# Performance work log

Hardware: AMD Instinct MI355X
Metric: run time of the kernel (lower is better)

The kernel has to match this reference:

```python
import jax, jax.numpy as jnp
import numpy as np
from jax import lax

B, C, H, W = 8, 64, 256, 256
K = 10  # num_experts


def conv1x1(x, w):
    # x: [B,C,H,W], w: [O,C] (1x1 conv, no bias)
    return jnp.einsum('oc,bchw->bohw', w, x)


def dyn_conv_se(x, attn, Wk, bk, gamma):
    # Dynamic_conv2d_se with with_se=True, kernel 3, stride 1, pad 1, groups=1.
    # attn: [B,K]; Wk: [K,O,I,3,3]; bk: [K,O]; gamma: [B,O]
    aw = jnp.einsum('bk,koihw->boihw', attn, Wk)        # per-sample kernels
    ab = attn @ bk                                      # [B,O]

    def one(xi, wi):
        # xi: [C,H,W], wi: [O,I,3,3]
        return lax.conv_general_dilated(
            xi[None], wi, window_strides=(1, 1), padding='SAME',
            dimension_numbers=('NCHW', 'OIHW', 'NCHW'))[0]

    y = jax.vmap(one)(x, aw) + ab[:, :, None, None]
    return y * gamma[:, :, None, None]  # SE gain


def setup_inputs() -> dict:
    key = jax.random.key(0)
    ks = jax.random.split(key, 12)
    x = jax.random.normal(ks[0], (B, C, H, W), dtype=jnp.float32)
    logits = jax.random.uniform(ks[1], (B, K), dtype=jnp.float32)
    weights = jax.nn.softmax(logits, axis=-1)
    gamma = jax.random.uniform(ks[2], (B, C), dtype=jnp.float32)
    par = jax.random.uniform(ks[3], (B, 3, 1, H, W), dtype=jnp.float32)
    s = 0.1  # default_init_weights scale
    w1 = jax.random.normal(ks[4], (K, C, C, 3, 3), dtype=jnp.float32) * s
    b1 = jax.random.normal(ks[5], (K, C), dtype=jnp.float32) * 0.01
    w2 = jax.random.normal(ks[6], (K, C, C, 3, 3), dtype=jnp.float32) * s
    b2 = jax.random.normal(ks[7], (K, C), dtype=jnp.float32) * 0.01
    w_16x16 = jax.random.normal(ks[8], (C, C), dtype=jnp.float32) * s
    w_16x8 = jax.random.normal(ks[9], (C, C), dtype=jnp.float32) * s
    w_8x8 = jax.random.normal(ks[10], (C, C), dtype=jnp.float32) * s
    return {'x': x, 'weights': weights, 'gamma': gamma, 'par': par,
            'w1': w1, 'b1': b1, 'w2': w2, 'b2': b2,
            'w_16x16': w_16x16, 'w_16x8': w_16x8, 'w_8x8': w_8x8}


def reference(x, weights, gamma, par, w1, b1, w2, b2, w_16x16, w_16x8, w_8x8):
    # channel_first=True, sparse_val=False, one_layer=False, res_scale=1
    identity = x
    dyres = (conv1x1(x, w_16x16) * par[:, 0]
             + conv1x1(x, w_16x8) * par[:, 1]
             + conv1x1(x, w_8x8) * par[:, 2])
    out = jax.nn.relu(dyn_conv_se(x, weights, w2, b2, gamma) + dyres)
    out = dyn_conv_se(out, weights, w1, b1, gamma)
    return identity + out  # res_scale = 1
```

## Files before the change

### kernel.cpp

```cpp
#include <hip/hip_runtime.h>
#include <hip/hip_bf16.h>

typedef __attribute__((ext_vector_type(8))) short short8;
typedef __attribute__((ext_vector_type(4))) float f32x4;

#define B_ 8
#define C_ 64
#define H_ 256
#define W_ 256
#define HW_ 65536
#define K_ 10
#define NS1 24
#define NS2 18
#define HP_ 258
#define WP_ 258
#define PXP_ (HP_*WP_)
#define SLABW 34
#define SLABR 10

static __device__ __forceinline__ unsigned short f2bf(float f) {
    __hip_bfloat16 hb = __float2bfloat16(f);
    return *(unsigned short*)&hb;
}
static __device__ __forceinline__ float bf2f(unsigned short u) {
    unsigned v = ((unsigned)u) << 16;
    float f;
    __builtin_memcpy(&f, &v, 4);
    return f;
}

static __device__ __forceinline__ void gload_lds16(const void* g, void* l) {
    __builtin_amdgcn_global_load_lds(
        (const __attribute__((address_space(1))) unsigned int*)(unsigned long long)g,
        (__attribute__((address_space(3))) unsigned int*)(unsigned int)(unsigned long long)l,
        16, 0, 0);
}

__global__ void k_combine(const float* __restrict__ attn, const float* __restrict__ gamma,
                          const float* __restrict__ w1, const float* __restrict__ b1,
                          const float* __restrict__ w2, const float* __restrict__ b2,
                          const float* __restrict__ w16, const float* __restrict__ w168,
                          const float* __restrict__ w88,
                          unsigned short* __restrict__ W4_1, unsigned short* __restrict__ W4_2,
                          float* __restrict__ bias1, float* __restrict__ bias2) {
    const int N1 = B_ * NS1 * 2048;
    const int N2 = B_ * NS2 * 2048;
    int gid = blockIdx.x * 256 + threadIdx.x;
    if (gid < N1) {
        int b = gid / (NS1 * 2048);
        int r = gid - b * (NS1 * 2048);
        int s = r >> 11;
        int r2 = r & 2047;
        int of = r2 >> 9, l = (r2 >> 3) & 63, j = r2 & 7;
        int o = of * 16 + (l & 15);
        int g = l >> 4;
        float val;
        if (s < 18) {
            int t = s >> 1, h = s & 1;
            int c = h * 32 + g * 8 + j;
            float acc = 0.f;
            #pragma unroll
            for (int k = 0; k < K_; ++k)
                acc += attn[b * K_ + k] * w2[((size_t)(k * 64 + o) * 64 + c) * 9 + t];
            val = acc * gamma[b * 64 + o];
        } else {
            int e = s - 18;
            int m = e >> 1, h = e & 1;
            int c = h * 32 + g * 8 + j;
            const float* wm = (m == 0) ? w16 : (m == 1 ? w168 : w88);
            val = wm[o * 64 + c];
        }
        W4_1[gid] = f2bf(val);
    } else if (gid < N1 + N2) {
        int gid2 = gid - N1;
        int b = gid2 / (NS2 * 2048);
        int r = gid2 - b * (NS2 * 2048);
        int s = r >> 11;
        int r2 = r & 2047;
        int of = r2 >> 9, l = (r2 >> 3) & 63, j = r2 & 7;
        int o = of * 16 + (l & 15);
        int g = l >> 4;
        int t = s >> 1, h = s & 1;
        int c = h * 32 + g * 8 + j;
        float acc = 0.f;
        #pragma unroll
        for (int k = 0; k < K_; ++k)
            acc += attn[b * K_ + k] * w1[((size_t)(k * 64 + o) * 64 + c) * 9 + t];
        W4_2[gid2] = f2bf(acc * gamma[b * 64 + o]);
    } else if (gid < N1 + N2 + 1024) {
        int id2 = gid - N1 - N2;
        int b = id2 >> 7;
        int rest = id2 & 127;
        int o = rest >> 1;
        int which = rest & 1;
        const float* bb = which ? b1 : b2;
        float acc = 0.f;
        #pragma unroll
        for (int k = 0; k < K_; ++k) acc += attn[b * K_ + k] * bb[k * 64 + o];
        float v = acc * gamma[b * 64 + o];
        if (which) bias2[b * 64 + o] = v; else bias1[b * 64 + o] = v;
    }
}

__global__ void k_border(unsigned short* __restrict__ X1p, unsigned short* __restrict__ Tp) {
    int gid = blockIdx.x * 256 + threadIdx.x;
    if (gid >= 2 * B_ * 1028 * 8) return;
    int chunk = gid & 7;
    int rest = gid >> 3;
    int p = rest % 1028;
    int rb = rest / 1028;
    int buf = rb & 1, b = rb >> 1;
    int row, col;
    if (p < 258) { row = 0; col = p; }
    else if (p < 516) { row = 257; col = p - 258; }
    else if (p < 772) { row = p - 516 + 1; col = 0; }
    else { row = p - 772 + 1; col = 257; }
    unsigned short* base = (buf ? Tp : X1p) +
        ((size_t)b * PXP_ + (size_t)row * WP_ + col) * 64 + chunk * 8;
    *(short8*)base = (short8){0, 0, 0, 0, 0, 0, 0, 0};
}

__global__ __launch_bounds__(256) void k_prep(const float* __restrict__ x,
                                              unsigned short* __restrict__ X1p) {
    __shared__ float ls[64][65];
    const int b = blockIdx.y;
    const int px0 = blockIdx.x * 64;
    const int row = px0 >> 8;
    const int col0 = px0 & 255;
    const int t = threadIdx.x;
    for (int e = t; e < 4096; e += 256) {
        int ch = e >> 6, px = e & 63;
        ls[ch][px] = x[((size_t)b * 64 + ch) * HW_ + px0 + px];
    }
    __syncthreads();
    unsigned short* dst = X1p + ((size_t)b * PXP_ + (size_t)(row + 1) * WP_ + col0 + 1) * 64;
    for (int e = t; e < 4096; e += 256) {
        int ch = e & 63, px = e >> 6;
        dst[(size_t)px * 64 + ch] = f2bf(ls[ch][px]);
    }
}

template<int STAGE>
__global__ __launch_bounds__(512, 4) void k_conv(
    const unsigned short* __restrict__ Xp,
    const float* __restrict__ x_res,
    const float* __restrict__ par,
    const unsigned short* __restrict__ W4,
    const float* __restrict__ bias,
    unsigned short* __restrict__ Tp,
    float* __restrict__ Fout)
{
    constexpr int NS = (STAGE == 1) ? NS1 : NS2;
    __shared__ short xs[SLABR * SLABW * 64];
    __shared__ short bring[5 * 2048];

    const int tid = threadIdx.x;
    const int l = tid & 63;
    const int wv = tid >> 6;
    const int r_local = (wv >> 2) * 4 + (wv & 3);
    const int b = blockIdx.y;
    const int bswz = (blockIdx.x & 7) * 32 + (blockIdx.x >> 3);
    const int rblk = bswz >> 3;
    const int cblk = bswz & 7;
    const int gh0 = rblk * 8, w0 = cblk * 32;
    const int ln15 = l & 15, g = l >> 4;

    const char* XbP = (const char*)Xp + (size_t)b * PXP_ * 128;
    const unsigned short* Wb = W4 + (size_t)b * (NS * 2048);

    float pvv[3][2];
    if constexpr (STAGE == 1) {
        #pragma unroll
        for (int m = 0; m < 3; ++m)
            #pragma unroll
            for (int mf = 0; mf < 2; ++mf)
                pvv[m][mf] = par[((size_t)b * 3 + m) * HW_ +
                                 (gh0 + r_local) * W_ + w0 + 16 * mf + ln15];
    }

    f32x4 acc[2][4];
    #pragma unroll
    for (int mf = 0; mf < 2; ++mf)
        #pragma unroll
        for (int of = 0; of < 4; ++of)
            acc[mf][of] = (f32x4){0.f, 0.f, 0.f, 0.f};

    #pragma unroll
    for (int it = 0; it < 6; ++it) {
        int tau = tid + it * 512;
        if (tau < SLABR * SLABW * 8) {
            int slot = tau & 7;
            int rest = tau >> 3;
            int px = rest % SLABW;
            int row = rest / SLABW;
            int cb = slot ^ (px & 7);
            gload_lds16(XbP + ((size_t)(gh0 + row) * WP_ + (w0 + px)) * 128 + cb * 16,
                        (char*)xs + (size_t)tau * 16);
        }
    }
    auto stage_b = [&](int s) {
        gload_lds16((const char*)Wb + (size_t)s * 4096 + tid * 16,
                    (char*)bring + (s % 5) * 4096 + tid * 16);
    };
    if (tid < 256) { stage_b(0); stage_b(1); stage_b(2); stage_b(3); }

    auto aload = [&](int s, short8* d) {
        const int t = s >> 1, h = s & 1;
        const int dh = t / 3, dw = t - 3 * dh;
        #pragma unroll
        for (int mf = 0; mf < 2; ++mf) {
            int idx = 16 * mf + ln15 + dw;
            d[mf] = *(const short8*)((const char*)xs +
                     ((r_local + dh) * SLABW + idx) * 128 +
                     ((((h << 2) | g) ^ (idx & 7)) << 4));
        }
    };

    if (wv < 4) asm volatile("s_waitcnt vmcnt(3)" ::: "memory");
    else        asm volatile("s_waitcnt vmcnt(0)" ::: "memory");
    __builtin_amdgcn_s_barrier();

    short8 aa[2][2];
    aload(0, aa[0]);

    #pragma unroll
    for (int s = 0; s < NS; ++s) {
        const char* rbase = (const char*)bring + (s % 5) * 4096 + (size_t)l * 16;
        short8 bf0 = *(const short8*)(rbase);
        short8 bf1 = *(const short8*)(rbase + 1024);
        short8 bf2 = *(const short8*)(rbase + 2048);
        short8 bf3 = *(const short8*)(rbase + 3072);
        if (s + 4 < NS && tid < 256) stage_b(s + 4);
        if (s + 1 < NS) {
            if (STAGE == 2 || s + 1 < 18) aload(s + 1, aa[(s + 1) & 1]);
            else aload(8 + ((s + 1) & 1), aa[(s + 1) & 1]);
        }
        short8 af[2];
        if (STAGE == 1 && s >= 18) {
            const int m = (s - 18) >> 1;
            #pragma unroll
            for (int mf = 0; mf < 2; ++mf)
                #pragma unroll
                for (int j = 0; j < 8; ++j)
                    af[mf][j] = (short)f2bf(bf2f((unsigned short)aa[s & 1][mf][j]) * pvv[m][mf]);
        } else {
            af[0] = aa[s & 1][0];
            af[1] = aa[s & 1][1];
        }
        #pragma unroll
        for (int mf = 0; mf < 2; ++mf) {
            acc[mf][0] = __builtin_amdgcn_mfma_f32_16x16x32_bf16(af[mf], bf0, acc[mf][0], 0, 0, 0);
            acc[mf][1] = __builtin_amdgcn_mfma_f32_16x16x32_bf16(af[mf], bf1, acc[mf][1], 0, 0, 0);
            acc[mf][2] = __builtin_amdgcn_mfma_f32_16x16x32_bf16(af[mf], bf2, acc[mf][2], 0, 0, 0);
            acc[mf][3] = __builtin_amdgcn_mfma_f32_16x16x32_bf16(af[mf], bf3, acc[mf][3], 0, 0, 0);
        }
        if (s + 1 < NS) {
            const int nw = (NS - 2 - s) < 3 ? (NS - 2 - s) : 3;
            if (nw == 3)      asm volatile("s_waitcnt vmcnt(3)" ::: "memory");
            else if (nw == 2) asm volatile("s_waitcnt vmcnt(2)" ::: "memory");
            else if (nw == 1) asm volatile("s_waitcnt vmcnt(1)" ::: "memory");
            else              asm volatile("s_waitcnt vmcnt(0)" ::: "memory");
            __builtin_amdgcn_s_barrier();
        }
    }

    if constexpr (STAGE == 1) {
        __syncthreads();
        unsigned short* tl = (unsigned short*)xs;
        #pragma unroll
        for (int of = 0; of < 4; ++of) {
            int o = of * 16 + ln15;
            float bi = bias[b * 64 + o];
            #pragma unroll
            for (int mf = 0; mf < 2; ++mf) {
                #pragma unroll
                for (int q = 0; q < 4; ++q) {
                    int px = 16 * mf + 4 * g + q;
                    float v = fmaxf(acc[mf][of][q] + bi, 0.f);
                    tl[r_local * 2048 + px * 64 + (o ^ ((px & 7) << 3))] = f2bf(v);
                }
            }
        }
        __syncthreads();
        #pragma unroll
        for (int it = 0; it < 4; ++it) {
            int tau = tid + it * 512;
            int row = tau >> 8;
            int px = (tau >> 3) & 31;
            int j = tau & 7;
            short8 v = *(const short8*)(tl + row * 2048 + px * 64 + ((j ^ (px & 7)) * 8));
            *(short8*)(Tp + ((size_t)b * PXP_ + (size_t)(gh0 + row + 1) * WP_ +
                             (w0 + 1 + px)) * 64 + j * 8) = v;
        }
    } else {
        const int gh = gh0 + r_local;
        #pragma unroll
        for (int of = 0; of < 4; ++of) {
            int o = of * 16 + ln15;
            float bi = bias[b * 64 + o];
            #pragma unroll
            for (int mf = 0; mf < 2; ++mf) {
                int gw = w0 + 16 * mf + g * 4;
                size_t idx = ((size_t)b * 64 + o) * HW_ + gh * W_ + gw;
                f32x4 xv = *(const f32x4*)(x_res + idx);
                f32x4 ov;
                #pragma unroll
                for (int q = 0; q < 4; ++q) ov[q] = xv[q] + acc[mf][of][q] + bi;
                *(f32x4*)(Fout + idx) = ov;
            }
        }
    }
}

extern "C" void kernel_launch(void* const* d_in, const int* in_sizes, int n_in,
                              void* d_out, int out_size, void* d_ws, size_t ws_size,
                              hipStream_t stream) {
    const float* x     = (const float*)d_in[0];
    const float* attn  = (const float*)d_in[1];
    const float* gamma = (const float*)d_in[2];
    const float* par   = (const float*)d_in[3];
    const float* w1    = (const float*)d_in[4];
    const float* b1    = (const float*)d_in[5];
    const float* w2    = (const float*)d_in[6];
    const float* b2    = (const float*)d_in[7];
    const float* w16   = (const float*)d_in[8];
    const float* w168  = (const float*)d_in[9];
    const float* w88   = (const float*)d_in[10];
    float* out = (float*)d_out;

    char* w = (char*)d_ws;
    unsigned short* W4_1 = (unsigned short*)w;
    unsigned short* W4_2 = (unsigned short*)(w + 786432);
    float* bias1 = (float*)(w + 786432 + 589824);
    float* bias2 = (float*)(w + 786432 + 589824 + 2048);
    unsigned short* X1p = (unsigned short*)(w + 1380352);
    unsigned short* Tp  = (unsigned short*)(w + 1380352 + 68161536);

    k_combine<<<dim3(2692), dim3(256), 0, stream>>>(attn, gamma, w1, b1, w2, b2,
                                                    w16, w168, w88, W4_1, W4_2, bias1, bias2);
    k_border<<<dim3(514), dim3(256), 0, stream>>>(X1p, Tp);
    k_prep<<<dim3(1024, 8), dim3(256), 0, stream>>>(x, X1p);

    dim3 grid(256, 8);
    k_conv<1><<<grid, dim3(512), 0, stream>>>(X1p, nullptr, par, W4_1, bias1, Tp, nullptr);
    k_conv<2><<<grid, dim3(512), 0, stream>>>(Tp, x, nullptr, W4_2, bias2, nullptr, out);
}
```

Measured before the change: 197.7 us.

## Halve conv block to 4 waves with 2x4 MFMA tiles per wave and paired k-steps

The conv kernel drops from 8 waves of 512 threads to 4 waves of 256 threads, and each wave now computes two image rows (a 4x4 grid of MFMA accumulators instead of 2x4). This doubles register-level reuse of every B fragment and halves the B fragments read from LDS per MFMA. The main loop handles two k-steps per barrier with a 6-deep weight ring buffer and raises wave priority around the MFMA bursts. In exchange, accumulator and register pressure is higher, there are fewer waves to hide latency, and every thread now issues the weight loads.

```diff
diff --git a/kernel.cpp b/kernel.cpp
--- a/kernel.cpp
+++ b/kernel.cpp
@@ -141,7 +141,7 @@
 }
 
 template<int STAGE>
-__global__ __launch_bounds__(512, 4) void k_conv(
+__global__ __launch_bounds__(256, 2) void k_conv(
     const unsigned short* __restrict__ Xp,
     const float* __restrict__ x_res,
     const float* __restrict__ par,
@@ -151,13 +151,13 @@
     float* __restrict__ Fout)
 {
     constexpr int NS = (STAGE == 1) ? NS1 : NS2;
+    constexpr int NPH = NS / 2;
     __shared__ short xs[SLABR * SLABW * 64];
-    __shared__ short bring[5 * 2048];
+    __shared__ short bring[6 * 2048];
 
     const int tid = threadIdx.x;
     const int l = tid & 63;
     const int wv = tid >> 6;
-    const int r_local = (wv >> 2) * 4 + (wv & 3);
     const int b = blockIdx.y;
     const int bswz = (blockIdx.x & 7) * 32 + (blockIdx.x >> 3);
     const int rblk = bswz >> 3;
@@ -168,26 +168,26 @@
     const char* XbP = (const char*)Xp + (size_t)b * PXP_ * 128;
     const unsigned short* Wb = W4 + (size_t)b * (NS * 2048);
 
-    float pvv[3][2];
+    float pvv[3][4];
     if constexpr (STAGE == 1) {
         #pragma unroll
         for (int m = 0; m < 3; ++m)
             #pragma unroll
-            for (int mf = 0; mf < 2; ++mf)
+            for (int mf = 0; mf < 4; ++mf)
                 pvv[m][mf] = par[((size_t)b * 3 + m) * HW_ +
-                                 (gh0 + r_local) * W_ + w0 + 16 * mf + ln15];
-    }
-
-    f32x4 acc[2][4];
+                                 (gh0 + 2 * wv + (mf >> 1)) * W_ + w0 + 16 * (mf & 1) + ln15];
+    }
+
+    f32x4 acc[4][4];
     #pragma unroll
-    for (int mf = 0; mf < 2; ++mf)
+    for (int mf = 0; mf < 4; ++mf)
         #pragma unroll
         for (int of = 0; of < 4; ++of)
             acc[mf][of] = (f32x4){0.f, 0.f, 0.f, 0.f};
 
     #pragma unroll
-    for (int it = 0; it < 6; ++it) {
-        int tau = tid + it * 512;
+    for (int it = 0; it < 11; ++it) {
+        int tau = tid + it * 256;
         if (tau < SLABR * SLABW * 8) {
             int slot = tau & 7;
             int rest = tau >> 3;
@@ -200,64 +200,71 @@
     }
     auto stage_b = [&](int s) {
         gload_lds16((const char*)Wb + (size_t)s * 4096 + tid * 16,
-                    (char*)bring + (s % 5) * 4096 + tid * 16);
+                    (char*)bring + (s % 6) * 4096 + tid * 16);
     };
-    if (tid < 256) { stage_b(0); stage_b(1); stage_b(2); stage_b(3); }
+    stage_b(0); stage_b(1); stage_b(2); stage_b(3);
 
     auto aload = [&](int s, short8* d) {
-        const int t = s >> 1, h = s & 1;
-        const int dh = t / 3, dw = t - 3 * dh;
-        #pragma unroll
-        for (int mf = 0; mf < 2; ++mf) {
-            int idx = 16 * mf + ln15 + dw;
-            d[mf] = *(const short8*)((const char*)xs +
-                     ((r_local + dh) * SLABW + idx) * 128 +
-                     ((((h << 2) | g) ^ (idx & 7)) << 4));
+        int dh, dw;
+        const int h = s & 1;
+        if (STAGE == 1 && s >= 18) { dh = 1; dw = 1; }
+        else { const int t = s >> 1; dh = t / 3; dw = t - 3 * dh; }
+        #pragma unroll
+        for (int mf = 0; mf < 4; ++mf) {
+            int idx = 16 * (mf & 1) + ln15 + dw;
+            int row = 2 * wv + (mf >> 1) + dh;
+            d[mf] = *(const short8*)((const char*)xs + (row * SLABW + idx) * 128 +
+                                     ((((h << 2) | g) ^ (idx & 7)) << 4));
         }
     };
 
-    if (wv < 4) asm volatile("s_waitcnt vmcnt(3)" ::: "memory");
-    else        asm volatile("s_waitcnt vmcnt(0)" ::: "memory");
+    asm volatile("s_waitcnt vmcnt(2)" ::: "memory");
     __builtin_amdgcn_s_barrier();
 
-    short8 aa[2][2];
-    aload(0, aa[0]);
-
     #pragma unroll
-    for (int s = 0; s < NS; ++s) {
-        const char* rbase = (const char*)bring + (s % 5) * 4096 + (size_t)l * 16;
-        short8 bf0 = *(const short8*)(rbase);
-        short8 bf1 = *(const short8*)(rbase + 1024);
-        short8 bf2 = *(const short8*)(rbase + 2048);
-        short8 bf3 = *(const short8*)(rbase + 3072);
-        if (s + 4 < NS && tid < 256) stage_b(s + 4);
-        if (s + 1 < NS) {
-            if (STAGE == 2 || s + 1 < 18) aload(s + 1, aa[(s + 1) & 1]);
-            else aload(8 + ((s + 1) & 1), aa[(s + 1) & 1]);
-        }
-        short8 af[2];
-        if (STAGE == 1 && s >= 18) {
-            const int m = (s - 18) >> 1;
-            #pragma unroll
-            for (int mf = 0; mf < 2; ++mf)
+    for (int p = 0; p < NPH; ++p) {
+        const int s0 = 2 * p, s1 = 2 * p + 1;
+        const char* r0 = (const char*)bring + (s0 % 6) * 4096 + (size_t)l * 16;
+        const char* r1 = (const char*)bring + (s1 % 6) * 4096 + (size_t)l * 16;
+        short8 b0[4], b1[4];
+        #pragma unroll
+        for (int of = 0; of < 4; ++of) {
+            b0[of] = *(const short8*)(r0 + of * 1024);
+            b1[of] = *(const short8*)(r1 + of * 1024);
+        }
+        short8 a0[4], a1[4];
+        aload(s0, a0);
+        aload(s1, a1);
+        if (s0 + 4 < NS) stage_b(s0 + 4);
+        if (s1 + 4 < NS) stage_b(s1 + 4);
+        if (STAGE == 1 && s0 >= 18) {
+            const int m = (s0 - 18) >> 1;
+            #pragma unroll
+            for (int mf = 0; mf < 4; ++mf)
                 #pragma unroll
-                for (int j = 0; j < 8; ++j)
-                    af[mf][j] = (short)f2bf(bf2f((unsigned short)aa[s & 1][mf][j]) * pvv[m][mf]);
-        } else {
-            af[0] = aa[s & 1][0];
-            af[1] = aa[s & 1][1];
-        }
-        #pragma unroll
-        for (int mf = 0; mf < 2; ++mf) {
-            acc[mf][0] = __builtin_amdgcn_mfma_f32_16x16x32_bf16(af[mf], bf0, acc[mf][0], 0, 0, 0);
-            acc[mf][1] = __builtin_amdgcn_mfma_f32_16x16x32_bf16(af[mf], bf1, acc[mf][1], 0, 0, 0);
-            acc[mf][2] = __builtin_amdgcn_mfma_f32_16x16x32_bf16(af[mf], bf2, acc[mf][2], 0, 0, 0);
-            acc[mf][3] = __builtin_amdgcn_mfma_f32_16x16x32_bf16(af[mf], bf3, acc[mf][3], 0, 0, 0);
-        }
-        if (s + 1 < NS) {
-            const int nw = (NS - 2 - s) < 3 ? (NS - 2 - s) : 3;
-            if (nw == 3)      asm volatile("s_waitcnt vmcnt(3)" ::: "memory");
-            else if (nw == 2) asm volatile("s_waitcnt vmcnt(2)" ::: "memory");
+                for (int j = 0; j < 8; ++j) {
+                    a0[mf][j] = (short)f2bf(bf2f((unsigned short)a0[mf][j]) * pvv[m][mf]);
+                    a1[mf][j] = (short)f2bf(bf2f((unsigned short)a1[mf][j]) * pvv[m][mf]);
+                }
+        }
+        __builtin_amdgcn_s_setprio(1);
+        #pragma unroll
+        for (int mf = 0; mf < 4; ++mf)
+            #pragma unroll
+            for (int of = 0; of < 4; ++of)
+                acc[mf][of] = __builtin_amdgcn_mfma_f32_16x16x32_bf16(
+                    a0[mf], b0[of], acc[mf][of], 0, 0, 0);
+        #pragma unroll
+        for (int mf = 0; mf < 4; ++mf)
+            #pragma unroll
+            for (int of = 0; of < 4; ++of)
+                acc[mf][of] = __builtin_amdgcn_mfma_f32_16x16x32_bf16(
+                    a1[mf], b1[of], acc[mf][of], 0, 0, 0);
+        __builtin_amdgcn_s_setprio(0);
+        if (p + 1 < NPH) {
+            const int rem = NS - (2 * p + 2);
+            const int nw = (rem >= 4) ? 2 : (rem - 2 > 0 ? rem - 2 : 0);
+            if (nw == 2)      asm volatile("s_waitcnt vmcnt(2)" ::: "memory");
             else if (nw == 1) asm volatile("s_waitcnt vmcnt(1)" ::: "memory");
             else              asm volatile("s_waitcnt vmcnt(0)" ::: "memory");
             __builtin_amdgcn_s_barrier();
@@ -272,19 +279,20 @@
             int o = of * 16 + ln15;
             float bi = bias[b * 64 + o];
             #pragma unroll
-            for (int mf = 0; mf < 2; ++mf) {
+            for (int mf = 0; mf < 4; ++mf) {
+                int row_local = 2 * wv + (mf >> 1);
                 #pragma unroll
                 for (int q = 0; q < 4; ++q) {
-                    int px = 16 * mf + 4 * g + q;
+                    int px = 16 * (mf & 1) + 4 * g + q;
                     float v = fmaxf(acc[mf][of][q] + bi, 0.f);
-                    tl[r_local * 2048 + px * 64 + (o ^ ((px & 7) << 3))] = f2bf(v);
+                    tl[row_local * 2048 + px * 64 + (o ^ ((px & 7) << 3))] = f2bf(v);
                 }
             }
         }
         __syncthreads();
         #pragma unroll
-        for (int it = 0; it < 4; ++it) {
-            int tau = tid + it * 512;
+        for (int it = 0; it < 8; ++it) {
+            int tau = tid + it * 256;
             int row = tau >> 8;
             int px = (tau >> 3) & 31;
             int j = tau & 7;
@@ -293,14 +301,14 @@
                              (w0 + 1 + px)) * 64 + j * 8) = v;
         }
     } else {
-        const int gh = gh0 + r_local;
         #pragma unroll
         for (int of = 0; of < 4; ++of) {
             int o = of * 16 + ln15;
             float bi = bias[b * 64 + o];
             #pragma unroll
-            for (int mf = 0; mf < 2; ++mf) {
-                int gw = w0 + 16 * mf + g * 4;
+            for (int mf = 0; mf < 4; ++mf) {
+                int gh = gh0 + 2 * wv + (mf >> 1);
+                int gw = w0 + 16 * (mf & 1) + g * 4;
                 size_t idx = ((size_t)b * 64 + o) * HW_ + gh * W_ + gw;
                 f32x4 xv = *(const f32x4*)(x_res + idx);
                 f32x4 ov;
@@ -342,6 +350,6 @@
     k_prep<<<dim3(1024, 8), dim3(256), 0, stream>>>(x, X1p);
 
     dim3 grid(256, 8);
-    k_conv<1><<<grid, dim3(512), 0, stream>>>(X1p, nullptr, par, W4_1, bias1, Tp, nullptr);
-    k_conv<2><<<grid, dim3(512), 0, stream>>>(Tp, x, nullptr, W4_2, bias2, nullptr, out);
-}
+    k_conv<1><<<grid, dim3(256), 0, stream>>>(X1p, nullptr, par, W4_1, bias1, Tp, nullptr);
+    k_conv<2><<<grid, dim3(256), 0, stream>>>(Tp, x, nullptr, W4_2, bias2, nullptr, out);
+}
```

After: 186.4 us. -5.7%, faster.
